# Optimization experiments

Hardware: AMD Instinct MI355X
Metric: run time of the kernel (lower is better)

The kernel has to match this reference:

```python
import jax, jax.numpy as jnp
import numpy as np
import math

D_MODEL = 1024
HEADS = 16
D_K = D_MODEL // HEADS
BATCH = 4
SEQ = 1024


def setup_inputs() -> dict:
    key = jax.random.key(0)
    ks = jax.random.split(key, 12)
    s = 1.0 / math.sqrt(D_MODEL)
    inp = {
        "q": jax.random.normal(ks[0], (BATCH, SEQ, D_MODEL), jnp.float32),
        "k": jax.random.normal(ks[1], (BATCH, SEQ, D_MODEL), jnp.float32),
        "v": jax.random.normal(ks[2], (BATCH, SEQ, D_MODEL), jnp.float32),
        # causal mask, broadcastable over (batch, heads)
        "mask": jnp.tril(jnp.ones((SEQ, SEQ), jnp.bool_))[None, None, :, :],
        "Wq": jax.random.normal(ks[3], (D_MODEL, D_MODEL), jnp.float32) * s,
        "bq": jax.random.normal(ks[4], (D_MODEL,), jnp.float32) * 0.01,
        "Wk": jax.random.normal(ks[5], (D_MODEL, D_MODEL), jnp.float32) * s,
        "bk": jax.random.normal(ks[6], (D_MODEL,), jnp.float32) * 0.01,
        "Wv": jax.random.normal(ks[7], (D_MODEL, D_MODEL), jnp.float32) * s,
        "bv": jax.random.normal(ks[8], (D_MODEL,), jnp.float32) * 0.01,
        "Wo": jax.random.normal(ks[9], (D_MODEL, D_MODEL), jnp.float32) * s,
        "bo": jax.random.normal(ks[10], (D_MODEL,), jnp.float32) * 0.01,
    }
    return inp


def reference(q, k, v, mask, Wq, bq, Wk, bk, Wv, bv, Wo, bo):
    B, S, _ = q.shape
    # projections (torch Linear: x @ W.T + b; here W stored as [in, out])
    def proj(x, W, b):
        return (x @ W + b).reshape(B, -1, HEADS, D_K).transpose(0, 2, 1, 3)

    Q = proj(q, Wq, bq)  # [B, H, S, Dk]
    K = proj(k, Wk, bk)
    V = proj(v, Wv, bv)

    scores = jnp.einsum("bhqd,bhkd->bhqk", Q, K) / math.sqrt(D_K)
    scores = jnp.where(mask, scores, jnp.float32(-1e9))
    attn = jax.nn.softmax(scores, axis=-1)  # dropout p=0.0 -> identity
    x = jnp.einsum("bhqk,bhkd->bhqd", attn, V)
    x = x.transpose(0, 2, 1, 3).reshape(B, S, D_MODEL)
    return x @ Wo + bo
```

## Files before the change

### kernel.cpp

```cpp
#include <hip/hip_runtime.h>
#include <math.h>

typedef __bf16 bf16_t;
typedef bf16_t bf16x8 __attribute__((ext_vector_type(8)));
typedef bf16_t bf16x4 __attribute__((ext_vector_type(4)));
typedef float  floatx4 __attribute__((ext_vector_type(4)));
typedef unsigned int u32;

#define MFMA_BF16(a, b, c) __builtin_amdgcn_mfma_f32_16x16x32_bf16((a), (b), (c), 0, 0, 0)

#if __has_builtin(__builtin_amdgcn_exp2f)
#define EXP2F(x) __builtin_amdgcn_exp2f(x)
#else
#define EXP2F(x) exp2f(x)
#endif

static constexpr int DMODEL = 1024;
static constexpr int NHEAD  = 16;
static constexpr int HDIM   = 64;
static constexpr int NBATCH = 4;
static constexpr int SEQLEN = 1024;
static constexpr int NTOK   = NBATCH * SEQLEN;

typedef __attribute__((address_space(3))) void       as3_void;
typedef __attribute__((address_space(1))) const void as1_cvoid;

__device__ __forceinline__ void gload16(const void* g, void* l) {
    __builtin_amdgcn_global_load_lds((as1_cvoid*)g, (as3_void*)l, 16, 0, 0);
}

__device__ __forceinline__ bf16x8 load_cvt8(const float* __restrict__ p) {
    floatx4 a = *(const floatx4*)p;
    floatx4 b = *(const floatx4*)(p + 4);
    bf16x8 r;
    r[0] = (bf16_t)a[0]; r[1] = (bf16_t)a[1]; r[2] = (bf16_t)a[2]; r[3] = (bf16_t)a[3];
    r[4] = (bf16_t)b[0]; r[5] = (bf16_t)b[1]; r[6] = (bf16_t)b[2]; r[7] = (bf16_t)b[3];
    return r;
}

__global__ __launch_bounds__(256) void prep(
    const float* __restrict__ W0, const float* __restrict__ W1,
    const float* __restrict__ W2, const float* __restrict__ W3,
    const float* __restrict__ q, const float* __restrict__ k, const float* __restrict__ v,
    bf16_t* __restrict__ Wt, bf16_t* __restrict__ Xr)
{
    __shared__ float tile[32][33];
    const int z = blockIdx.z;
    if (z < 4) {
        const float* W = (z == 0) ? W0 : (z == 1) ? W1 : (z == 2) ? W2 : W3;
        bf16_t* O = Wt + (size_t)z * DMODEL * DMODEL;
        const int tx = threadIdx.x & 31, ty = threadIdx.x >> 5;
        const int r0 = blockIdx.x * 32, c0 = blockIdx.y * 32;
#pragma unroll
        for (int i = 0; i < 32; i += 8)
            tile[ty + i][tx] = W[(size_t)(r0 + ty + i) * DMODEL + c0 + tx];
        __syncthreads();
#pragma unroll
        for (int i = 0; i < 32; i += 8)
            O[(size_t)(c0 + ty + i) * DMODEL + r0 + tx] = (bf16_t)tile[tx][ty + i];
    } else {
        const float* src = (z == 4) ? q : (z == 5) ? k : v;
        bf16_t* dst = Xr + (size_t)(z - 4) * ((size_t)NTOK * DMODEL);
        size_t i = (((size_t)blockIdx.y * 32 + blockIdx.x) * 256 + threadIdx.x) * 16;
        *(bf16x8*)(dst + i)     = load_cvt8(src + i);
        *(bf16x8*)(dst + i + 8) = load_cvt8(src + i + 8);
    }
}

__global__ __launch_bounds__(256) void transpose_w(
    const float* __restrict__ W0, const float* __restrict__ W1,
    const float* __restrict__ W2, const float* __restrict__ W3,
    bf16_t* __restrict__ out)
{
    __shared__ float tile[32][33];
    const float* W = (blockIdx.z == 0) ? W0 : (blockIdx.z == 1) ? W1
                   : (blockIdx.z == 2) ? W2 : W3;
    bf16_t* O = out + (size_t)blockIdx.z * DMODEL * DMODEL;
    int tx = threadIdx.x, ty = threadIdx.y;
    int r0 = blockIdx.x * 32, c0 = blockIdx.y * 32;
#pragma unroll
    for (int i = 0; i < 32; i += 8)
        tile[ty + i][tx] = W[(size_t)(r0 + ty + i) * DMODEL + c0 + tx];
    __syncthreads();
#pragma unroll
    for (int i = 0; i < 32; i += 8)
        O[(size_t)(c0 + ty + i) * DMODEL + r0 + tx] = (bf16_t)tile[tx][ty + i];
}
__global__ __launch_bounds__(256) void cvt_bf16(
    const float* __restrict__ src, bf16_t* __restrict__ dst)
{
    size_t i = ((size_t)blockIdx.x * 256 + threadIdx.x) * 8;
    *(bf16x8*)(dst + i) = load_cvt8(src + i);
}

__global__ __launch_bounds__(256) void gemm_qkv(
    const bf16_t* __restrict__ Xb, size_t astride, int mode0,
    const bf16_t* __restrict__ Wt,
    const float* __restrict__ bq, const float* __restrict__ bk, const float* __restrict__ bv,
    bf16_t* __restrict__ Qh, bf16_t* __restrict__ Kh, bf16_t* __restrict__ Vt)
{
    const int mode = mode0 + blockIdx.z;
    const bf16_t* A = Xb + astride * (size_t)blockIdx.z;
    const bf16_t* B = Wt + (size_t)mode * DMODEL * DMODEL;
    const float* bias = (mode == 0) ? bq : (mode == 1) ? bk : bv;
    bf16_t* out       = (mode == 0) ? Qh : (mode == 1) ? Kh : Vt;

    __shared__ __align__(16) bf16_t lA[3][128 * 32];
    __shared__ __align__(16) bf16_t lB[3][128 * 32];

    const int wave = threadIdx.x >> 6, lane = threadIdx.x & 63;
    const int quad = lane >> 4, l15 = lane & 15;
    const int wm = wave >> 1, wn = wave & 1;
    const int row0 = blockIdx.x * 128, col0 = blockIdx.y * 128;
    const int srow = lane >> 2;
    const int csrc = ((lane & 3) ^ ((lane >> 3) & 3)) * 8;
    const int pq8  = (quad ^ ((l15 >> 1) & 3)) * 8;

    const floatx4 zero = {0.f, 0.f, 0.f, 0.f};
    floatx4 acc[4][4];
#pragma unroll
    for (int mt = 0; mt < 4; mt++)
#pragma unroll
        for (int nt = 0; nt < 4; nt++) acc[mt][nt] = zero;

    const bf16_t* Abase = A + (size_t)(row0 + srow) * DMODEL + csrc;
    const bf16_t* Bbase = B + (size_t)(col0 + srow) * DMODEL + csrc;

#pragma unroll
    for (int p = 0; p < 2; p++) {
#pragma unroll
        for (int j = 0; j < 2; j++) {
            const int seg = j * 4 + wave;
            gload16(Abase + (size_t)seg * 16 * DMODEL + p * 32, lA[p] + seg * 512);
            gload16(Bbase + (size_t)seg * 16 * DMODEL + p * 32, lB[p] + seg * 512);
        }
    }

#pragma unroll
    for (int it = 0; it < 32; it++) {
        if (it < 31) asm volatile("s_waitcnt vmcnt(4)" ::: "memory");
        else         asm volatile("s_waitcnt vmcnt(0)" ::: "memory");
        __builtin_amdgcn_s_barrier();
        __builtin_amdgcn_sched_barrier(0);
        const int cur = it % 3;
        if (it + 2 < 32) {
            const int k2 = (it + 2) * 32;
            const int nb = (it + 2) % 3;
#pragma unroll
            for (int j = 0; j < 2; j++) {
                const int seg = j * 4 + wave;
                gload16(Abase + (size_t)seg * 16 * DMODEL + k2, lA[nb] + seg * 512);
                gload16(Bbase + (size_t)seg * 16 * DMODEL + k2, lB[nb] + seg * 512);
            }
        }
        bf16x8 aF[4], bF[4];
#pragma unroll
        for (int t = 0; t < 4; t++) {
            aF[t] = *(const bf16x8*)(lA[cur] + (wm * 64 + t * 16 + l15) * 32 + pq8);
            bF[t] = *(const bf16x8*)(lB[cur] + (wn * 64 + t * 16 + l15) * 32 + pq8);
        }
#pragma unroll
        for (int mt = 0; mt < 4; mt++)
#pragma unroll
            for (int nt = 0; nt < 4; nt++)
                acc[mt][nt] = MFMA_BF16(bF[nt], aF[mt], acc[mt][nt]);
    }

    const int hh = (col0 + wn * 64) >> 6;
#pragma unroll
    for (int nt = 0; nt < 4; nt++) {
        const int gn0 = col0 + wn * 64 + nt * 16 + quad * 4;
        const floatx4 bb = *(const floatx4*)&bias[gn0];
        const int dd0 = (wn * 64 + nt * 16 + quad * 4) & 63;
#pragma unroll
        for (int mt = 0; mt < 4; mt++) {
            const int tok = row0 + wm * 64 + mt * 16 + l15;
            const int b = tok >> 10, s = tok & 1023;
            if (mode == 2) {
#pragma unroll
                for (int r = 0; r < 4; r++)
                    Vt[((size_t)((b * NHEAD + hh) * HDIM + dd0 + r)) * SEQLEN + s] =
                        (bf16_t)(acc[mt][nt][r] + bb[r]);
            } else {
                bf16x4 v;
#pragma unroll
                for (int r = 0; r < 4; r++) {
                    float vv = acc[mt][nt][r] + bb[r];
                    if (mode == 0) vv *= 0.1803368801111204f;
                    v[r] = (bf16_t)vv;
                }
                *(bf16x4*)&out[((size_t)((b * NHEAD + hh) * SEQLEN + s)) * HDIM + dd0] = v;
            }
        }
    }
}

__global__ __launch_bounds__(256) void gemm_o(
    const bf16_t* __restrict__ Xa, const bf16_t* __restrict__ Wt,
    const float* __restrict__ bias, float* __restrict__ out)
{
    __shared__ __align__(16) bf16_t lA[3][64 * 32];
    __shared__ __align__(16) bf16_t lB[3][128 * 32];

    const int wave = threadIdx.x >> 6, lane = threadIdx.x & 63;
    const int quad = lane >> 4, l15 = lane & 15;
    const int wm = wave & 1, wn = wave >> 1;
    const int row0 = blockIdx.x * 64, col0 = blockIdx.y * 128;
    const int srow = lane >> 2;
    const int csrc = ((lane & 3) ^ ((lane >> 3) & 3)) * 8;
    const int pq8  = (quad ^ ((l15 >> 1) & 3)) * 8;

    const floatx4 zero = {0.f, 0.f, 0.f, 0.f};
    floatx4 acc[2][4];
#pragma unroll
    for (int mt = 0; mt < 2; mt++)
#pragma unroll
        for (int nt = 0; nt < 4; nt++) acc[mt][nt] = zero;

    const bf16_t* Abase = Xa + (size_t)(row0 + srow) * DMODEL + csrc;
    const bf16_t* Bbase = Wt + (size_t)(col0 + srow) * DMODEL + csrc;

#pragma unroll
    for (int p = 0; p < 2; p++) {
        gload16(Abase + (size_t)wave * 16 * DMODEL + p * 32, lA[p] + wave * 512);
#pragma unroll
        for (int j = 0; j < 2; j++) {
            const int seg = wave * 2 + j;
            gload16(Bbase + (size_t)seg * 16 * DMODEL + p * 32, lB[p] + seg * 512);
        }
    }

#pragma unroll
    for (int it = 0; it < 32; it++) {
        if (it < 31) asm volatile("s_waitcnt vmcnt(3)" ::: "memory");
        else         asm volatile("s_waitcnt vmcnt(0)" ::: "memory");
        __builtin_amdgcn_s_barrier();
        __builtin_amdgcn_sched_barrier(0);
        const int cur = it % 3;
        if (it + 2 < 32) {
            const int k2 = (it + 2) * 32;
            const int nb = (it + 2) % 3;
            gload16(Abase + (size_t)wave * 16 * DMODEL + k2, lA[nb] + wave * 512);
#pragma unroll
            for (int j = 0; j < 2; j++) {
                const int seg = wave * 2 + j;
                gload16(Bbase + (size_t)seg * 16 * DMODEL + k2, lB[nb] + seg * 512);
            }
        }
        bf16x8 aF[2], bF[4];
#pragma unroll
        for (int t = 0; t < 2; t++)
            aF[t] = *(const bf16x8*)(lA[cur] + (wm * 32 + t * 16 + l15) * 32 + pq8);
#pragma unroll
        for (int t = 0; t < 4; t++)
            bF[t] = *(const bf16x8*)(lB[cur] + (wn * 64 + t * 16 + l15) * 32 + pq8);
#pragma unroll
        for (int mt = 0; mt < 2; mt++)
#pragma unroll
            for (int nt = 0; nt < 4; nt++)
                acc[mt][nt] = MFMA_BF16(bF[nt], aF[mt], acc[mt][nt]);
    }

#pragma unroll
    for (int nt = 0; nt < 4; nt++) {
        const int gn0 = col0 + wn * 64 + nt * 16 + quad * 4;
        const floatx4 bb = *(const floatx4*)&bias[gn0];
#pragma unroll
        for (int mt = 0; mt < 2; mt++) {
            const int tok = row0 + wm * 32 + mt * 16 + l15;
            floatx4 v;
#pragma unroll
            for (int r = 0; r < 4; r++) v[r] = acc[mt][nt][r] + bb[r];
            *(floatx4*)&out[(size_t)tok * DMODEL + gn0] = v;
        }
    }
}

#define SHUF_PV(pk, Vv, oacc) do {                                                     \
    u32 a0 = __shfl(pk.u[0], srcA), a1 = __shfl(pk.u[1], srcA);                        \
    u32 a2 = __shfl(pk.u[0], srcB), a3 = __shfl(pk.u[1], srcB);                        \
    u32 b0 = __shfl(pk.u[2], srcA), b1 = __shfl(pk.u[3], srcA);                        \
    u32 b2 = __shfl(pk.u[2], srcB), b3 = __shfl(pk.u[3], srcB);                        \
    union { u32 u[4]; bf16x8 v; } bP;                                                  \
    bP.u[0] = hiP ? b0 : a0; bP.u[1] = hiP ? b1 : a1;                                  \
    bP.u[2] = hiP ? b2 : a2; bP.u[3] = hiP ? b3 : a3;                                  \
    __builtin_amdgcn_s_setprio(1);                                                     \
    _Pragma("unroll") for (int dt = 0; dt < 4; dt++)                                   \
        oacc[dt] = MFMA_BF16(Vv[dt], bP.v, oacc[dt]);                                  \
    __builtin_amdgcn_s_setprio(0);                                                     \
} while (0)

#define SOFTMAX_PV_FAST(S0x, S1x, Vv, lacc, oacc) do {                                 \
    float ps = 0.f;                                                                    \
    union { bf16_t hh2[8]; u32 u[4]; } pk;                                             \
    _Pragma("unroll") for (int r = 0; r < 4; r++) {                                    \
        float e0 = EXP2F(S0x[r]), e1 = EXP2F(S1x[r]);                                  \
        ps += e0 + e1;                                                                 \
        pk.hh2[r] = (bf16_t)e0; pk.hh2[4 + r] = (bf16_t)e1;                            \
    }                                                                                  \
    lacc += ps;                                                                        \
    SHUF_PV(pk, Vv, oacc);                                                             \
} while (0)

#define SOFTMAX_PV_MASK(S0x, S1x, Vv, kbv, qrow, lacc, oacc) do {                      \
    float ps = 0.f;                                                                    \
    union { bf16_t hh2[8]; u32 u[4]; } pk;                                             \
    _Pragma("unroll") for (int r = 0; r < 4; r++) {                                    \
        const int key0 = (kbv) + quad * 4 + r;                                         \
        float s0 = (key0 <= (qrow))      ? S0x[r] : -1e30f;                            \
        float s1 = (key0 + 16 <= (qrow)) ? S1x[r] : -1e30f;                            \
        float e0 = EXP2F(s0), e1 = EXP2F(s1);                                          \
        ps += e0 + e1;                                                                 \
        pk.hh2[r] = (bf16_t)e0; pk.hh2[4 + r] = (bf16_t)e1;                            \
    }                                                                                  \
    lacc += ps;                                                                        \
    SHUF_PV(pk, Vv, oacc);                                                             \
} while (0)

#define LOAD_KV(K0v, K1v, Vv, kbv) do {                                                \
    _Pragma("unroll") for (int c = 0; c < 2; c++) {                                    \
        K0v[c] = *(const bf16x8*)(Kp + (size_t)((kbv) + l15) * HDIM + c * 32 + quad * 8);      \
        K1v[c] = *(const bf16x8*)(Kp + (size_t)((kbv) + 16 + l15) * HDIM + c * 32 + quad * 8); \
    }                                                                                  \
    _Pragma("unroll") for (int dt = 0; dt < 4; dt++)                                   \
        Vv[dt] = *(const bf16x8*)(Vp + (size_t)(dt * 16 + l15) * SEQLEN + (kbv) + quad * 8);   \
} while (0)

__global__ __launch_bounds__(256, 2) void attn(
    const bf16_t* __restrict__ Qh, const bf16_t* __restrict__ Kh,
    const bf16_t* __restrict__ Vt, bf16_t* __restrict__ X)
{
    __shared__ __align__(8) float comb[2][64][68];
    const int wave = threadIdx.x >> 6, lane = threadIdx.x & 63;
    const int quad = lane >> 4, l15 = lane & 15;
    const int L = blockIdx.x;
    const int bh = (L & 7) * 8 + ((L >> 3) & 7);
    const int j  = L >> 6;
    const int b = bh >> 4, h = bh & 15;

    const int qbase0 = 32 * j,        qbase1 = 32 * j + 16;
    const int qbase2 = 992 - 32 * j,  qbase3 = 1008 - 32 * j;
    const int qrow0 = qbase0 + l15, qrow1 = qbase1 + l15;
    const int qrow2 = qbase2 + l15, qrow3 = qbase3 + l15;
    const int NKA = j + 1, NKB = 32 - j;

    const bf16_t* Qp = Qh + (size_t)bh * SEQLEN * HDIM;
    const bf16_t* Kp = Kh + (size_t)bh * SEQLEN * HDIM;
    const bf16_t* Vp = Vt + (size_t)bh * HDIM * SEQLEN;

    bf16x8 bQ0[2], bQ1[2], bQ2[2], bQ3[2];
#pragma unroll
    for (int c = 0; c < 2; c++) {
        bQ0[c] = *(const bf16x8*)(Qp + (size_t)qrow0 * HDIM + c * 32 + quad * 8);
        bQ1[c] = *(const bf16x8*)(Qp + (size_t)qrow1 * HDIM + c * 32 + quad * 8);
        bQ2[c] = *(const bf16x8*)(Qp + (size_t)qrow2 * HDIM + c * 32 + quad * 8);
        bQ3[c] = *(const bf16x8*)(Qp + (size_t)qrow3 * HDIM + c * 32 + quad * 8);
    }

    const floatx4 zero = {0.f, 0.f, 0.f, 0.f};
    float l0_ = 0.f, l1_ = 0.f, l2_ = 0.f, l3_ = 0.f;
    floatx4 o0[4], o1[4], o2[4], o3[4];
#pragma unroll
    for (int dt = 0; dt < 4; dt++) { o0[dt] = zero; o1[dt] = zero; o2[dt] = zero; o3[dt] = zero; }

    const int srcA = ((quad & 1) ? 32 : 0) + l15;
    const int srcB = srcA + 16;
    const bool hiP = (quad >= 2);

    for (int kc = wave; kc < NKB; kc += 4) {
        const int kb = kc * 32;
        bf16x8 K0[2], K1[2], Vv[4];
        LOAD_KV(K0, K1, Vv, kb);

        const bool doA = (kc < NKA);
        floatx4 S0_0 = zero, S1_0 = zero, S0_1 = zero, S1_1 = zero;
        floatx4 S0_2 = zero, S1_2 = zero, S0_3 = zero, S1_3 = zero;
        __builtin_amdgcn_s_setprio(1);
#pragma unroll
        for (int c = 0; c < 2; c++) {
            S0_2 = MFMA_BF16(K0[c], bQ2[c], S0_2);
            S1_2 = MFMA_BF16(K1[c], bQ2[c], S1_2);
            S0_3 = MFMA_BF16(K0[c], bQ3[c], S0_3);
            S1_3 = MFMA_BF16(K1[c], bQ3[c], S1_3);
        }
        __builtin_amdgcn_s_setprio(0);
        if (doA) {
            __builtin_amdgcn_s_setprio(1);
#pragma unroll
            for (int c = 0; c < 2; c++) {
                S0_0 = MFMA_BF16(K0[c], bQ0[c], S0_0);
                S1_0 = MFMA_BF16(K1[c], bQ0[c], S1_0);
                S0_1 = MFMA_BF16(K0[c], bQ1[c], S0_1);
                S1_1 = MFMA_BF16(K1[c], bQ1[c], S1_1);
            }
            __builtin_amdgcn_s_setprio(0);
        }
        if (kb + 31 <= qbase2) { SOFTMAX_PV_FAST(S0_2, S1_2, Vv, l2_, o2); }
        else                   { SOFTMAX_PV_MASK(S0_2, S1_2, Vv, kb, qrow2, l2_, o2); }
        if (kb + 31 <= qbase3) { SOFTMAX_PV_FAST(S0_3, S1_3, Vv, l3_, o3); }
        else                   { SOFTMAX_PV_MASK(S0_3, S1_3, Vv, kb, qrow3, l3_, o3); }
        if (doA) {
            if (kb + 31 <= qbase0) { SOFTMAX_PV_FAST(S0_0, S1_0, Vv, l0_, o0); }
            else                   { SOFTMAX_PV_MASK(S0_0, S1_0, Vv, kb, qrow0, l0_, o0); }
            if (kb + 31 <= qbase1) { SOFTMAX_PV_FAST(S0_1, S1_1, Vv, l1_, o1); }
            else                   { SOFTMAX_PV_MASK(S0_1, S1_1, Vv, kb, qrow1, l1_, o1); }
        }
    }

    auto publish = [&](int slot) {
        float2* d2 = (float2*)&comb[slot][lane][0];
#pragma unroll
        for (int dt = 0; dt < 4; dt++) {
            d2[ 0 + 2 * dt]     = make_float2(o0[dt][0], o0[dt][1]);
            d2[ 0 + 2 * dt + 1] = make_float2(o0[dt][2], o0[dt][3]);
            d2[ 8 + 2 * dt]     = make_float2(o1[dt][0], o1[dt][1]);
            d2[ 8 + 2 * dt + 1] = make_float2(o1[dt][2], o1[dt][3]);
            d2[16 + 2 * dt]     = make_float2(o2[dt][0], o2[dt][1]);
            d2[16 + 2 * dt + 1] = make_float2(o2[dt][2], o2[dt][3]);
            d2[24 + 2 * dt]     = make_float2(o3[dt][0], o3[dt][1]);
            d2[24 + 2 * dt + 1] = make_float2(o3[dt][2], o3[dt][3]);
        }
        d2[32] = make_float2(l0_, l1_);
        d2[33] = make_float2(l2_, l3_);
    };
    auto accum = [&](int slot) {
        const float2* s2 = (const float2*)&comb[slot][lane][0];
#pragma unroll
        for (int dt = 0; dt < 4; dt++) {
            float2 p0 = s2[ 0 + 2 * dt], p1 = s2[ 0 + 2 * dt + 1];
            float2 q0 = s2[ 8 + 2 * dt], q1 = s2[ 8 + 2 * dt + 1];
            float2 r0 = s2[16 + 2 * dt], r1 = s2[16 + 2 * dt + 1];
            float2 t0 = s2[24 + 2 * dt], t1 = s2[24 + 2 * dt + 1];
            o0[dt][0] += p0.x; o0[dt][1] += p0.y; o0[dt][2] += p1.x; o0[dt][3] += p1.y;
            o1[dt][0] += q0.x; o1[dt][1] += q0.y; o1[dt][2] += q1.x; o1[dt][3] += q1.y;
            o2[dt][0] += r0.x; o2[dt][1] += r0.y; o2[dt][2] += r1.x; o2[dt][3] += r1.y;
            o3[dt][0] += t0.x; o3[dt][1] += t0.y; o3[dt][2] += t1.x; o3[dt][3] += t1.y;
        }
        float2 la = s2[32], lb = s2[33];
        l0_ += la.x; l1_ += la.y; l2_ += lb.x; l3_ += lb.y;
    };

    if (wave & 1) publish(wave >> 1);
    __syncthreads();
    if (!(wave & 1)) accum(wave >> 1);
    __syncthreads();
    if (wave == 2) publish(0);
    __syncthreads();
    if (wave == 0) {
        accum(0);

        l0_ += __shfl_xor(l0_, 16); l0_ += __shfl_xor(l0_, 32);
        l1_ += __shfl_xor(l1_, 16); l1_ += __shfl_xor(l1_, 32);
        l2_ += __shfl_xor(l2_, 16); l2_ += __shfl_xor(l2_, 32);
        l3_ += __shfl_xor(l3_, 16); l3_ += __shfl_xor(l3_, 32);

        const float i0 = 1.f / l0_, i1 = 1.f / l1_, i2 = 1.f / l2_, i3 = 1.f / l3_;
#pragma unroll
        for (int dt = 0; dt < 4; dt++) {
            bf16x4 v0, v1, v2, v3;
#pragma unroll
            for (int r = 0; r < 4; r++) {
                v0[r] = (bf16_t)(o0[dt][r] * i0);
                v1[r] = (bf16_t)(o1[dt][r] * i1);
                v2[r] = (bf16_t)(o2[dt][r] * i2);
                v3[r] = (bf16_t)(o3[dt][r] * i3);
            }
            const size_t cofs = (size_t)h * HDIM + dt * 16 + quad * 4;
            *(bf16x4*)(&X[((size_t)(b * SEQLEN + qrow0)) * DMODEL + cofs]) = v0;
            *(bf16x4*)(&X[((size_t)(b * SEQLEN + qrow1)) * DMODEL + cofs]) = v1;
            *(bf16x4*)(&X[((size_t)(b * SEQLEN + qrow2)) * DMODEL + cofs]) = v2;
            *(bf16x4*)(&X[((size_t)(b * SEQLEN + qrow3)) * DMODEL + cofs]) = v3;
        }
    }
}

extern "C" void kernel_launch(void* const* d_in, const int* in_sizes, int n_in,
                              void* d_out, int out_size, void* d_ws, size_t ws_size,
                              hipStream_t stream)
{
    const float* q  = (const float*)d_in[0];
    const float* k  = (const float*)d_in[1];
    const float* v  = (const float*)d_in[2];
    const float* Wq = (const float*)d_in[4];
    const float* bq = (const float*)d_in[5];
    const float* Wk = (const float*)d_in[6];
    const float* bk = (const float*)d_in[7];
    const float* Wv = (const float*)d_in[8];
    const float* bv = (const float*)d_in[9];
    const float* Wo = (const float*)d_in[10];
    const float* bo = (const float*)d_in[11];
    float* out = (float*)d_out;

    char* ws = (char*)d_ws;
    const size_t MB = 1ull << 20;
    const size_t NELEM = (size_t)NTOK * DMODEL;
    bf16_t* Wt = (bf16_t*)ws;
    bf16_t* Qh = (bf16_t*)(ws + 8 * MB);
    bf16_t* Kh = (bf16_t*)(ws + 16 * MB);
    bf16_t* Vt = (bf16_t*)(ws + 24 * MB);
    bf16_t* Xr = (bf16_t*)(ws + 32 * MB);

    if (ws_size >= 56 * MB) {
        prep<<<dim3(32, 32, 7), dim3(256), 0, stream>>>(Wq, Wk, Wv, Wo, q, k, v, Wt, Xr);
        gemm_qkv<<<dim3(32, 8, 3), dim3(256), 0, stream>>>(
            Xr, NELEM, 0, Wt, bq, bk, bv, Qh, Kh, Vt);
    } else {
        transpose_w<<<dim3(32, 32, 4), dim3(32, 8), 0, stream>>>(Wq, Wk, Wv, Wo, Wt);
        const float* qkv_in[3] = {q, k, v};
        for (int m = 0; m < 3; m++) {
            cvt_bf16<<<dim3(2048), dim3(256), 0, stream>>>(qkv_in[m], Xr);
            gemm_qkv<<<dim3(32, 8, 1), dim3(256), 0, stream>>>(
                Xr, 0, m, Wt, bq, bk, bv, Qh, Kh, Vt);
        }
    }

    bf16_t* Xa = Xr;
    attn<<<dim3(1024), dim3(256), 0, stream>>>(Qh, Kh, Vt, Xa);
    gemm_o<<<dim3(64, 8), dim3(256), 0, stream>>>(
        Xa, Wt + 3 * (size_t)DMODEL * DMODEL, bo, out);
}
```

Before: 209.8 us.

## Store Q/K/V in MFMA-fragment-tiled layout for contiguous per-lane attention loads

```diff
diff --git a/kernel.cpp b/kernel.cpp
--- a/kernel.cpp
+++ b/kernel.cpp
@@ -171,17 +171,27 @@
     for (int nt = 0; nt < 4; nt++) {
         const int gn0 = col0 + wn * 64 + nt * 16 + quad * 4;
         const floatx4 bb = *(const floatx4*)&bias[gn0];
-        const int dd0 = (wn * 64 + nt * 16 + quad * 4) & 63;
+        const int dd0 = gn0 & 63;
 #pragma unroll
         for (int mt = 0; mt < 4; mt++) {
             const int tok = row0 + wm * 64 + mt * 16 + l15;
             const int b = tok >> 10, s = tok & 1023;
+            const int bh = b * NHEAD + hh;
             if (mode == 2) {
+                const int kc = s >> 5;
+                const int dt = (dd0 >> 4) & 3;
+                const int quadA = (s >> 3) & 3;
+                const int e = s & 7;
+                bf16_t* vb = Vt + ((size_t)(bh * 32 + kc) * 4 + dt) * 512
+                                + quadA * 128 + (dd0 & 15) * 8 + e;
 #pragma unroll
                 for (int r = 0; r < 4; r++)
-                    Vt[((size_t)((b * NHEAD + hh) * HDIM + dd0 + r)) * SEQLEN + s] =
-                        (bf16_t)(acc[mt][nt][r] + bb[r]);
+                    vb[r * 8] = (bf16_t)(acc[mt][nt][r] + bb[r]);
             } else {
+                const int t16 = s >> 4;
+                const int c = dd0 >> 5;
+                const int quadA = (dd0 >> 3) & 3;
+                const int e0 = dd0 & 7;
                 bf16x4 v;
 #pragma unroll
                 for (int r = 0; r < 4; r++) {
@@ -189,7 +199,8 @@
                     if (mode == 0) vv *= 0.1803368801111204f;
                     v[r] = (bf16_t)vv;
                 }
-                *(bf16x4*)&out[((size_t)((b * NHEAD + hh) * SEQLEN + s)) * HDIM + dd0] = v;
+                *(bf16x4*)&out[((size_t)(bh * 128 + t16 * 2 + c)) * 512
+                               + quadA * 128 + l15 * 8 + e0] = v;
             }
         }
     }
@@ -317,13 +328,13 @@
     SHUF_PV(pk, Vv, oacc);                                                             \
 } while (0)
 
-#define LOAD_KV(K0v, K1v, Vv, kbv) do {                                                \
+#define LOAD_KV(K0v, K1v, Vv, kcv) do {                                                \
     _Pragma("unroll") for (int c = 0; c < 2; c++) {                                    \
-        K0v[c] = *(const bf16x8*)(Kp + (size_t)((kbv) + l15) * HDIM + c * 32 + quad * 8);      \
-        K1v[c] = *(const bf16x8*)(Kp + (size_t)((kbv) + 16 + l15) * HDIM + c * 32 + quad * 8); \
+        K0v[c] = *(const bf16x8*)(Kp + ((size_t)(kcv) * 4 + c) * 512 + lane * 8);      \
+        K1v[c] = *(const bf16x8*)(Kp + ((size_t)(kcv) * 4 + 2 + c) * 512 + lane * 8);  \
     }                                                                                  \
     _Pragma("unroll") for (int dt = 0; dt < 4; dt++)                                   \
-        Vv[dt] = *(const bf16x8*)(Vp + (size_t)(dt * 16 + l15) * SEQLEN + (kbv) + quad * 8);   \
+        Vv[dt] = *(const bf16x8*)(Vp + ((size_t)(kcv) * 4 + dt) * 512 + lane * 8);     \
 } while (0)
 
 __global__ __launch_bounds__(256, 2) void attn(
@@ -344,17 +355,17 @@
     const int qrow2 = qbase2 + l15, qrow3 = qbase3 + l15;
     const int NKA = j + 1, NKB = 32 - j;
 
-    const bf16_t* Qp = Qh + (size_t)bh * SEQLEN * HDIM;
-    const bf16_t* Kp = Kh + (size_t)bh * SEQLEN * HDIM;
-    const bf16_t* Vp = Vt + (size_t)bh * HDIM * SEQLEN;
+    const bf16_t* Qp = Qh + (size_t)bh * 65536;
+    const bf16_t* Kp = Kh + (size_t)bh * 65536;
+    const bf16_t* Vp = Vt + (size_t)bh * 65536;
 
     bf16x8 bQ0[2], bQ1[2], bQ2[2], bQ3[2];
 #pragma unroll
     for (int c = 0; c < 2; c++) {
-        bQ0[c] = *(const bf16x8*)(Qp + (size_t)qrow0 * HDIM + c * 32 + quad * 8);
-        bQ1[c] = *(const bf16x8*)(Qp + (size_t)qrow1 * HDIM + c * 32 + quad * 8);
-        bQ2[c] = *(const bf16x8*)(Qp + (size_t)qrow2 * HDIM + c * 32 + quad * 8);
-        bQ3[c] = *(const bf16x8*)(Qp + (size_t)qrow3 * HDIM + c * 32 + quad * 8);
+        bQ0[c] = *(const bf16x8*)(Qp + ((size_t)(qbase0 >> 4) * 2 + c) * 512 + lane * 8);
+        bQ1[c] = *(const bf16x8*)(Qp + ((size_t)(qbase1 >> 4) * 2 + c) * 512 + lane * 8);
+        bQ2[c] = *(const bf16x8*)(Qp + ((size_t)(qbase2 >> 4) * 2 + c) * 512 + lane * 8);
+        bQ3[c] = *(const bf16x8*)(Qp + ((size_t)(qbase3 >> 4) * 2 + c) * 512 + lane * 8);
     }
 
     const floatx4 zero = {0.f, 0.f, 0.f, 0.f};
@@ -370,7 +381,7 @@
     for (int kc = wave; kc < NKB; kc += 4) {
         const int kb = kc * 32;
         bf16x8 K0[2], K1[2], Vv[4];
-        LOAD_KV(K0, K1, Vv, kb);
+        LOAD_KV(K0, K1, Vv, kc);
 
         const bool doA = (kc < NKA);
         floatx4 S0_0 = zero, S1_0 = zero, S0_1 = zero, S1_1 = zero;
```

Result: faster. 198.1 us (-5.6%).
